# Kernel optimization log

Hardware: AMD Instinct MI355X
Metric: run time of the kernel (lower is better)

Reference implementation:

```python
import jax, jax.numpy as jnp
import numpy as np

B, S, D = 8, 1024, 1024
H = 16
DH = D // H
DFF = 4096
L = 2
EPS = 1e-6


def setup_inputs() -> dict:
    key = jax.random.key(0)
    ks = jax.random.split(key, 12)
    sc = 0.02
    x = jax.random.normal(ks[0], (B, S, D), dtype=jnp.float32)
    # causal mask: 1 where position j > i (masked), broadcast over batch/head
    mask = jnp.triu(jnp.ones((S, S), dtype=jnp.float32), k=1)[None, None]
    Wq = jax.random.normal(ks[1], (L, D, D), dtype=jnp.float32) * sc
    Wk = jax.random.normal(ks[2], (L, D, D), dtype=jnp.float32) * sc
    Wv = jax.random.normal(ks[3], (L, D, D), dtype=jnp.float32) * sc
    Wo = jax.random.normal(ks[4], (L, D, D), dtype=jnp.float32) * sc
    bq = jnp.zeros((L, D), jnp.float32)
    bk = jnp.zeros((L, D), jnp.float32)
    bv = jnp.zeros((L, D), jnp.float32)
    bo = jnp.zeros((L, D), jnp.float32)
    W1 = jax.random.normal(ks[5], (L, D, DFF), dtype=jnp.float32) * sc
    b1 = jnp.zeros((L, DFF), jnp.float32)
    W2 = jax.random.normal(ks[6], (L, DFF, D), dtype=jnp.float32) * sc
    b2 = jnp.zeros((L, D), jnp.float32)
    ln1_g = jnp.ones((L, D), jnp.float32)
    ln1_b = jnp.zeros((L, D), jnp.float32)
    ln2_g = jnp.ones((L, D), jnp.float32)
    ln2_b = jnp.zeros((L, D), jnp.float32)
    return dict(x=x, mask=mask, Wq=Wq, bq=bq, Wk=Wk, bk=bk, Wv=Wv, bv=bv,
                Wo=Wo, bo=bo, W1=W1, b1=b1, W2=W2, b2=b2,
                ln1_g=ln1_g, ln1_b=ln1_b, ln2_g=ln2_g, ln2_b=ln2_b)


def layer_norm(x, g, b):
    mu = jnp.mean(x, axis=-1, keepdims=True)
    var = jnp.mean(jnp.square(x - mu), axis=-1, keepdims=True)
    return (x - mu) * jax.lax.rsqrt(var + EPS) * g + b


def reference(x, mask, Wq, bq, Wk, bk, Wv, bv, Wo, bo, W1, b1, W2, b2,
              ln1_g, ln1_b, ln2_g, ln2_b):
    scale = 1.0 / jnp.sqrt(jnp.float32(DH))
    for l in range(L):
        # --- multi-head attention (inference mode: no dropout) ---
        q = (x @ Wq[l] + bq[l]).reshape(B, S, H, DH).transpose(0, 2, 1, 3)
        k = (x @ Wk[l] + bk[l]).reshape(B, S, H, DH).transpose(0, 2, 1, 3)
        v = (x @ Wv[l] + bv[l]).reshape(B, S, H, DH).transpose(0, 2, 1, 3)
        sim = jnp.einsum('bhqd,bhkd->bhqk', q, k) * scale + mask * (-1e9)
        attn = jax.nn.softmax(sim, axis=-1)
        o = jnp.einsum('bhqk,bhkd->bhqd', attn, v)
        o = o.transpose(0, 2, 1, 3).reshape(B, S, D)
        o = o @ Wo[l] + bo[l]
        x = layer_norm(o + x, ln1_g[l], ln1_b[l])
        # --- feed-forward network ---
        h = jax.nn.relu(x @ W1[l] + b1[l])
        f = h @ W2[l] + b2[l]
        x = layer_norm(x + f, ln2_g[l], ln2_b[l])
    return x
```

## Files before the change

kernel.cpp:

```cpp
#include <hip/hip_runtime.h>

typedef __attribute__((ext_vector_type(8))) short bf16x8;
typedef __attribute__((ext_vector_type(4))) float f32x4;
typedef unsigned short ushort_t;
typedef unsigned int uint32;

#define DEV __device__ __forceinline__

DEV ushort_t f2bf(float f) {
    uint32 u = __float_as_uint(f);
    uint32 r = (u + 0x7FFFu + ((u >> 16) & 1u)) >> 16;
    return (ushort_t)r;
}

#define MFMA16(a, b, c) __builtin_amdgcn_mfma_f32_16x16x32_bf16((a), (b), (c), 0, 0, 0)

DEV void gload_lds16(const void* g, void* l) {
    __builtin_amdgcn_global_load_lds((const __attribute__((address_space(1))) void*)g,
                                     (__attribute__((address_space(3))) void*)l,
                                     16, 0, 0);
}

__global__ __launch_bounds__(256) void init_x(const float* __restrict__ xin,
                                              float* __restrict__ x,
                                              ushort_t* __restrict__ xb, int n4) {
    int i = blockIdx.x * 256 + threadIdx.x;
    if (i >= n4) return;
    float4 v = ((const float4*)xin)[i];
    ((float4*)x)[i] = v;
    ushort4 h;
    h.x = f2bf(v.x); h.y = f2bf(v.y); h.z = f2bf(v.z); h.w = f2bf(v.w);
    ((ushort4*)xb)[i] = h;
}

__global__ __launch_bounds__(256) void transpose_convert(const float* __restrict__ src,
                                                         ushort_t* __restrict__ dst,
                                                         int K, int N) {
    __shared__ float tile[32][33];
    int tx = threadIdx.x, ty = threadIdx.y;
    int nt = blockIdx.x * 32, kt = blockIdx.y * 32;
#pragma unroll
    for (int j = 0; j < 4; ++j)
        tile[ty + j * 8][tx] = src[(size_t)(kt + ty + j * 8) * N + nt + tx];
    __syncthreads();
#pragma unroll
    for (int j = 0; j < 4; ++j)
        dst[(size_t)(nt + ty + j * 8) * K + kt + tx] = f2bf(tile[tx][ty + j * 8]);
}

template <int BM, int MODE, int RELU>
__global__ __launch_bounds__(512, 2) void gemm8p(const ushort_t* __restrict__ A,
                                                 const ushort_t* __restrict__ BT,
                                                 const float* __restrict__ bias,
                                                 void* __restrict__ Cout,
                                                 int M, int N, int K, int gx,
                                                 ushort_t* __restrict__ qout,
                                                 ushort_t* __restrict__ kout,
                                                 ushort_t* __restrict__ vtout,
                                                 const float* __restrict__ bq,
                                                 const float* __restrict__ bk,
                                                 const float* __restrict__ bv) {
    constexpr int AH = BM / 128;
    constexpr int MREP = BM / 32;
    constexpr int MPP = MREP / 4;
    __shared__ ushort_t lds[2][(BM + 256) * 64];

    const int nwg = gridDim.x;
    const int q8 = nwg >> 3, r8 = nwg & 7;
    const int xcd = blockIdx.x & 7, idx = blockIdx.x >> 3;
    const int swz = (xcd < r8 ? xcd * (q8 + 1) : r8 * (q8 + 1) + (xcd - r8) * q8) + idx;
    const int bxi = swz % gx, byi = swz / gx;

    const int tid = threadIdx.x;
    const int w = tid >> 6, lane = tid & 63;
    const int wr = w >> 2, wc = w & 3;
    const int lr = lane & 15, lh = lane >> 4;
    const int row0 = byi * BM, col0 = bxi * 256;

    f32x4 acc[MREP][4] = {};

    const ushort_t* __restrict__ Ab = A + (size_t)row0 * K;
    const ushort_t* __restrict__ Bb = BT + (size_t)col0 * K;
    const int nt = K >> 6;

    const int sr8 = lane & 7;
    const int r8l = lane >> 3;
    const int cu = (lane & 7) ^ r8l;

    auto stage_half = [&](const ushort_t* src, ushort_t* lbase) {
#pragma unroll
        for (int i = 0; i < 2; ++i) {
            const int rowi = (w * 2 + i) * 8 + r8l;
            gload_lds16(src + (size_t)rowi * K + cu * 8, lbase + (w * 2 + i) * 512 + lane * 8);
        }
    };
    auto Ahalf = [&](int buf, int h) -> ushort_t* { return &lds[buf][h * 8192]; };
    auto Bhalf = [&](int buf, int h) -> ushort_t* { return &lds[buf][BM * 64 + h * 8192]; };
    auto stA = [&](int kt, int h, int buf) {
        stage_half(Ab + (size_t)h * 128 * K + (size_t)kt * 64, Ahalf(buf, h));
    };
    auto stB = [&](int kt, int h, int buf) {
        stage_half(Bb + (size_t)h * 128 * K + (size_t)kt * 64, Bhalf(buf, h));
    };

    stB(0, 0, 0); stB(0, 1, 0);
    stA(0, 0, 0); if (AH == 2) stA(0, 1, 0);
    stB(1, 0, 1); stB(1, 1, 1);
    asm volatile("s_waitcnt vmcnt(4)" ::: "memory");
    __builtin_amdgcn_sched_barrier(0);
    __builtin_amdgcn_s_barrier();

    for (int t = 0; t < nt; ++t) {
        const int cb = t & 1, nb = cb ^ 1;
        bf16x8 bfrag[4][2];
#pragma unroll
        for (int p = 0; p < 4; ++p) {
            if (p == 0) {
#pragma unroll
                for (int ni = 0; ni < 4; ++ni) {
                    const int br = wc * 64 + ni * 16 + lr;
                    const ushort_t* bh = Bhalf(cb, br >> 7);
                    const int rr = br & 127;
#pragma unroll
                    for (int ks = 0; ks < 2; ++ks)
                        bfrag[ni][ks] = *(const bf16x8*)&bh[rr * 64 + (((ks * 4 + lh) ^ (rr & 7)) * 8)];
                }
            }
            bf16x8 af[MPP][2];
#pragma unroll
            for (int mm = 0; mm < MPP; ++mm) {
                const int fr = wr * (BM / 2) + (p * MPP + mm) * 16 + lr;
                const ushort_t* ah = Ahalf(cb, fr >> 7);
                const int rr = fr & 127;
#pragma unroll
                for (int ks = 0; ks < 2; ++ks)
                    af[mm][ks] = *(const bf16x8*)&ah[rr * 64 + (((ks * 4 + lh) ^ (rr & 7)) * 8)];
            }
            if (p == 0) { if (t + 1 < nt) stA(t + 1, 0, nb); }
            else if (p == 1) { if (AH == 2 && t + 1 < nt) stA(t + 1, 1, nb); }
            else if (p == 2) { if (t + 2 < nt) stB(t + 2, 0, cb); }
            else {
                if (t + 2 < nt) {
                    stB(t + 2, 1, cb);
                    asm volatile("s_waitcnt vmcnt(4)" ::: "memory");
                } else if (t + 1 < nt) {
                    asm volatile("s_waitcnt vmcnt(0)" ::: "memory");
                }
            }
            __builtin_amdgcn_sched_barrier(0);
            __builtin_amdgcn_s_barrier();
            asm volatile("s_waitcnt lgkmcnt(0)" ::: "memory");
            __builtin_amdgcn_sched_barrier(0);
            __builtin_amdgcn_s_setprio(1);
#pragma unroll
            for (int mm = 0; mm < MPP; ++mm)
#pragma unroll
                for (int ni = 0; ni < 4; ++ni)
#pragma unroll
                    for (int ks = 0; ks < 2; ++ks)
                        acc[p * MPP + mm][ni] = MFMA16(af[mm][ks], bfrag[ni][ks], acc[p * MPP + mm][ni]);
            __builtin_amdgcn_s_setprio(0);
            __builtin_amdgcn_sched_barrier(0);
            __builtin_amdgcn_s_barrier();
        }
    }
    (void)sr8; (void)M;

#pragma unroll
    for (int mi = 0; mi < MREP; ++mi) {
#pragma unroll
        for (int ni = 0; ni < 4; ++ni) {
            const int col = col0 + wc * 64 + ni * 16 + lr;
            const int rowb = row0 + wr * (BM / 2) + mi * 16 + lh * 4;
            if (MODE == 2) {
                if (col < 1024) {
                    const float bvv = bq[col];
#pragma unroll
                    for (int r = 0; r < 4; ++r)
                        qout[(size_t)(rowb + r) * 1024 + col] = f2bf((acc[mi][ni][r] + bvv) * 0.125f);
                } else if (col < 2048) {
                    const int c = col - 1024;
                    const float bvv = bk[c];
#pragma unroll
                    for (int r = 0; r < 4; ++r)
                        kout[(size_t)(rowb + r) * 1024 + c] = f2bf(acc[mi][ni][r] + bvv);
                } else {
                    const int d = col - 2048;
                    const int h = d >> 6, dd = d & 63;
                    const int b = rowb >> 10, s = rowb & 1023;
                    const float bvv = bv[d];
                    ushort4 h4;
                    h4.x = f2bf(acc[mi][ni][0] + bvv);
                    h4.y = f2bf(acc[mi][ni][1] + bvv);
                    h4.z = f2bf(acc[mi][ni][2] + bvv);
                    h4.w = f2bf(acc[mi][ni][3] + bvv);
                    *(ushort4*)&vtout[(((size_t)(b * 16 + h) * 64 + dd) << 10) + s] = h4;
                }
            } else {
                const float bvv = bias[col];
#pragma unroll
                for (int r = 0; r < 4; ++r) {
                    float val = acc[mi][ni][r] + bvv;
                    if (RELU) val = fmaxf(val, 0.f);
                    if (MODE == 1)
                        ((ushort_t*)Cout)[(size_t)(rowb + r) * N + col] = f2bf(val);
                    else
                        ((float*)Cout)[(size_t)(rowb + r) * N + col] = val;
                }
            }
        }
    }
}

__global__ __launch_bounds__(256) void attn_kernel(const ushort_t* __restrict__ q,
                                                   const ushort_t* __restrict__ k,
                                                   const ushort_t* __restrict__ vt,
                                                   ushort_t* __restrict__ o) {
    __shared__ ushort_t ktile[64 * 64];
    __shared__ ushort_t vtile[64 * 64];
    __shared__ ushort_t p_lds[4][16 * 64];

    const int bh = blockIdx.x;
    const int b = bh >> 4, h = bh & 15;
    const int qt = blockIdx.y;
    const int tid = threadIdx.x, w = tid >> 6, lane = tid & 63;
    const int lr = lane & 15, lh = lane >> 4;
    const int qbase = qt * 64 + w * 16;
    const size_t headoff = (size_t)b * 1024 * 1024 + h * 64;
    const size_t vhead = (size_t)(b * 16 + h) << 16;

    bf16x8 qf[2];
#pragma unroll
    for (int ks = 0; ks < 2; ++ks)
        qf[ks] = *(const bf16x8*)&q[headoff + (size_t)(qbase + lr) * 1024 + ks * 32 + lh * 8];

    f32x4 oacc[4] = {};
    float m[4] = {-INFINITY, -INFINITY, -INFINITY, -INFINITY};
    float ls[4] = {0.f, 0.f, 0.f, 0.f};

    const int srow = tid >> 3;
    const int scolb = (tid & 7) * 16;
    const int swz0 = ((srow & 7) << 4);
    char* const kbase = (char*)ktile;
    char* const vbase = (char*)vtile;
    char* const kw0 = kbase + srow * 128 + (scolb ^ swz0);
    char* const kw1 = kbase + (srow + 32) * 128 + (scolb ^ swz0);
    char* const vw0 = vbase + srow * 128 + (scolb ^ swz0);
    char* const vw1 = vbase + (srow + 32) * 128 + (scolb ^ swz0);
    const ushort_t* kg = k + headoff + (size_t)srow * 1024 + (tid & 7) * 8;
    const ushort_t* vg = vt + vhead + (size_t)srow * 1024 + (tid & 7) * 8;

    const int jmaxw = qbase + 15;
    const int jend = qt * 64 + 63;

    bf16x8 sk0 = *(const bf16x8*)&kg[0];
    bf16x8 sk1 = *(const bf16x8*)&kg[32 * 1024];
    bf16x8 sv0 = *(const bf16x8*)&vg[0];
    bf16x8 sv1 = *(const bf16x8*)&vg[32 * 1024];

    for (int j0 = 0; j0 <= jend; j0 += 64) {
        __syncthreads();
        *(bf16x8*)kw0 = sk0;
        *(bf16x8*)kw1 = sk1;
        *(bf16x8*)vw0 = sv0;
        *(bf16x8*)vw1 = sv1;
        __syncthreads();
        if (j0 + 64 <= jend) {
            sk0 = *(const bf16x8*)&kg[(size_t)(j0 + 64) * 1024];
            sk1 = *(const bf16x8*)&kg[(size_t)(j0 + 64) * 1024 + 32 * 1024];
            sv0 = *(const bf16x8*)&vg[j0 + 64];
            sv1 = *(const bf16x8*)&vg[32 * 1024 + j0 + 64];
        }

        if (j0 <= jmaxw) {
            f32x4 s[4] = {{0,0,0,0},{0,0,0,0},{0,0,0,0},{0,0,0,0}};
#pragma unroll
            for (int kt = 0; kt < 4; ++kt) {
                const int row = kt * 16 + lr;
                const int rswz = ((row & 7) << 4);
#pragma unroll
                for (int ks = 0; ks < 2; ++ks) {
                    bf16x8 kf = *(const bf16x8*)(kbase + row * 128 + ((ks * 64 + lh * 16) ^ rswz));
                    s[kt] = MFMA16(qf[ks], kf, s[kt]);
                }
            }
            if (j0 + 63 > qbase) {
#pragma unroll
                for (int kt = 0; kt < 4; ++kt)
#pragma unroll
                    for (int r = 0; r < 4; ++r)
                        s[kt][r] = ((j0 + kt * 16 + lr) <= (qbase + lh * 4 + r)) ? s[kt][r] : -1e9f;
            }
#pragma unroll
            for (int r = 0; r < 4; ++r) {
                float pm = fmaxf(fmaxf(s[0][r], s[1][r]), fmaxf(s[2][r], s[3][r]));
                pm = fmaxf(pm, __shfl_xor(pm, 1, 16));
                pm = fmaxf(pm, __shfl_xor(pm, 2, 16));
                pm = fmaxf(pm, __shfl_xor(pm, 4, 16));
                pm = fmaxf(pm, __shfl_xor(pm, 8, 16));
                const float mn = fmaxf(m[r], pm);
                const float corr = __expf(m[r] - mn);
                m[r] = mn;
                float p0 = __expf(s[0][r] - mn);
                float p1 = __expf(s[1][r] - mn);
                float p2 = __expf(s[2][r] - mn);
                float p3 = __expf(s[3][r] - mn);
                s[0][r] = p0; s[1][r] = p1; s[2][r] = p2; s[3][r] = p3;
                float ps = (p0 + p1) + (p2 + p3);
                ps += __shfl_xor(ps, 1, 16);
                ps += __shfl_xor(ps, 2, 16);
                ps += __shfl_xor(ps, 4, 16);
                ps += __shfl_xor(ps, 8, 16);
                ls[r] = ls[r] * corr + ps;
                oacc[0][r] *= corr; oacc[1][r] *= corr;
                oacc[2][r] *= corr; oacc[3][r] *= corr;
            }
            char* const pb = (char*)p_lds[w];
#pragma unroll
            for (int r = 0; r < 4; ++r) {
                const int qrow = lh * 4 + r;
                const int qswz = ((qrow & 7) << 4);
#pragma unroll
                for (int kt = 0; kt < 4; ++kt)
                    *(ushort_t*)(pb + qrow * 128 + ((kt * 32 + lr * 2) ^ qswz)) = f2bf(s[kt][r]);
            }
            const int pswz = ((lr & 7) << 4);
            bf16x8 pa0 = *(const bf16x8*)(pb + lr * 128 + ((lh * 16) ^ pswz));
            bf16x8 pa1 = *(const bf16x8*)(pb + lr * 128 + ((64 + lh * 16) ^ pswz));
#pragma unroll
            for (int dt = 0; dt < 4; ++dt) {
                const int vrow = dt * 16 + lr;
                const int vswz = ((vrow & 7) << 4);
                bf16x8 vf0 = *(const bf16x8*)(vbase + vrow * 128 + ((lh * 16) ^ vswz));
                oacc[dt] = MFMA16(pa0, vf0, oacc[dt]);
                bf16x8 vf1 = *(const bf16x8*)(vbase + vrow * 128 + ((64 + lh * 16) ^ vswz));
                oacc[dt] = MFMA16(pa1, vf1, oacc[dt]);
            }
        }
    }

    float inv[4];
#pragma unroll
    for (int r = 0; r < 4; ++r) inv[r] = 1.f / ls[r];
#pragma unroll
    for (int dt = 0; dt < 4; ++dt)
#pragma unroll
        for (int r = 0; r < 4; ++r) {
            const int row = qbase + lh * 4 + r;
            o[headoff + (size_t)row * 1024 + dt * 16 + lr] = f2bf(oacc[dt][r] * inv[r]);
        }
}

__global__ __launch_bounds__(256) void add_ln(const float* __restrict__ t,
                                              float* __restrict__ x,
                                              const float* __restrict__ g,
                                              const float* __restrict__ bb,
                                              ushort_t* __restrict__ xb) {
    const int row = blockIdx.x, tid = threadIdx.x;
    const int lane = tid & 63, w = tid >> 6;
    const size_t base = (size_t)row * 1024;
    float4 tv = ((const float4*)(t + base))[tid];
    float4 xv = ((const float4*)(x + base))[tid];
    float v0 = tv.x + xv.x, v1 = tv.y + xv.y, v2 = tv.z + xv.z, v3 = tv.w + xv.w;
    float s = v0 + v1 + v2 + v3;
    float sq = v0 * v0 + v1 * v1 + v2 * v2 + v3 * v3;
#pragma unroll
    for (int off = 32; off >= 1; off >>= 1) {
        s += __shfl_xor(s, off);
        sq += __shfl_xor(sq, off);
    }
    __shared__ float red[8];
    if (lane == 0) { red[w] = s; red[4 + w] = sq; }
    __syncthreads();
    s = red[0] + red[1] + red[2] + red[3];
    sq = red[4] + red[5] + red[6] + red[7];
    const float mu = s * (1.f / 1024.f);
    const float var = sq * (1.f / 1024.f) - mu * mu;
    const float rs = rsqrtf(var + 1e-6f);
    float4 gv = ((const float4*)g)[tid];
    float4 bv = ((const float4*)bb)[tid];
    float y0 = (v0 - mu) * rs * gv.x + bv.x;
    float y1 = (v1 - mu) * rs * gv.y + bv.y;
    float y2 = (v2 - mu) * rs * gv.z + bv.z;
    float y3 = (v3 - mu) * rs * gv.w + bv.w;
    float4 yo; yo.x = y0; yo.y = y1; yo.z = y2; yo.w = y3;
    ((float4*)(x + base))[tid] = yo;
    ushort4 hh;
    hh.x = f2bf(y0); hh.y = f2bf(y1); hh.z = f2bf(y2); hh.w = f2bf(y3);
    ((ushort4*)(xb + base))[tid] = hh;
}

extern "C" void kernel_launch(void* const* d_in, const int* in_sizes, int n_in,
                              void* d_out, int out_size, void* d_ws, size_t ws_size,
                              hipStream_t stream) {
    (void)in_sizes; (void)n_in; (void)out_size; (void)ws_size;
    const int B = 8, S = 1024, D = 1024, DFF = 4096, L = 2;
    const int M = B * S;

    const float* x_in = (const float*)d_in[0];
    const float* Wq = (const float*)d_in[2];
    const float* bq = (const float*)d_in[3];
    const float* Wk = (const float*)d_in[4];
    const float* bk = (const float*)d_in[5];
    const float* Wv = (const float*)d_in[6];
    const float* bv = (const float*)d_in[7];
    const float* Wo = (const float*)d_in[8];
    const float* bo = (const float*)d_in[9];
    const float* W1 = (const float*)d_in[10];
    const float* b1 = (const float*)d_in[11];
    const float* W2 = (const float*)d_in[12];
    const float* b2 = (const float*)d_in[13];
    const float* ln1g = (const float*)d_in[14];
    const float* ln1b = (const float*)d_in[15];
    const float* ln2g = (const float*)d_in[16];
    const float* ln2b = (const float*)d_in[17];

    float* x = (float*)d_out;
    char* ws = (char*)d_ws;
    const size_t MB = 1024 * 1024;
    ushort_t* wqkvT = (ushort_t*)(ws + 0 * MB);
    ushort_t* woT = (ushort_t*)(ws + 12 * MB);
    ushort_t* w1T = (ushort_t*)(ws + 16 * MB);
    ushort_t* w2T = (ushort_t*)(ws + 32 * MB);
    ushort_t* xb  = (ushort_t*)(ws + 48 * MB);
    ushort_t* qb  = (ushort_t*)(ws + 64 * MB);
    ushort_t* kb  = (ushort_t*)(ws + 80 * MB);
    ushort_t* vtb = (ushort_t*)(ws + 96 * MB);
    ushort_t* ob  = (ushort_t*)(ws + 112 * MB);
    ushort_t* hb  = (ushort_t*)(ws + 64 * MB);
    float* t      = (float*)(ws + 128 * MB);

    init_x<<<M * D / 4 / 256, 256, 0, stream>>>(x_in, x, xb, M * D / 4);

    dim3 tb(32, 8);
    for (int l = 0; l < L; ++l) {
        const size_t wOff = (size_t)l * D * D;
        const size_t qkvOff = (size_t)l * 3 * D * D;
        transpose_convert<<<dim3(D / 32, D / 32), tb, 0, stream>>>(Wq + wOff, wqkvT + qkvOff, D, D);
        transpose_convert<<<dim3(D / 32, D / 32), tb, 0, stream>>>(Wk + wOff, wqkvT + qkvOff + (size_t)D * D, D, D);
        transpose_convert<<<dim3(D / 32, D / 32), tb, 0, stream>>>(Wv + wOff, wqkvT + qkvOff + 2 * (size_t)D * D, D, D);
        transpose_convert<<<dim3(D / 32, D / 32), tb, 0, stream>>>(Wo + wOff, woT + wOff, D, D);
        transpose_convert<<<dim3(DFF / 32, D / 32), tb, 0, stream>>>(W1 + (size_t)l * D * DFF, w1T + (size_t)l * D * DFF, D, DFF);
        transpose_convert<<<dim3(D / 32, DFF / 32), tb, 0, stream>>>(W2 + (size_t)l * DFF * D, w2T + (size_t)l * DFF * D, DFF, D);
    }

    for (int l = 0; l < L; ++l) {
        const size_t wOff = (size_t)l * D * D;
        const size_t bOff = (size_t)l * D;
        gemm8p<256, 2, 0><<<dim3(384), 512, 0, stream>>>(
            xb, wqkvT + (size_t)l * 3 * D * D, nullptr, nullptr, M, 3 * D, D, 12,
            qb, kb, vtb, bq + bOff, bk + bOff, bv + bOff);
        attn_kernel<<<dim3(B * 16, S / 64), 256, 0, stream>>>(qb, kb, vtb, ob);
        gemm8p<128, 0, 0><<<dim3(256), 512, 0, stream>>>(
            ob, woT + wOff, bo + bOff, t, M, D, D, 4,
            nullptr, nullptr, nullptr, nullptr, nullptr, nullptr);
        add_ln<<<M, 256, 0, stream>>>(t, x, ln1g + bOff, ln1b + bOff, xb);
        gemm8p<256, 1, 1><<<dim3(512), 512, 0, stream>>>(
            xb, w1T + (size_t)l * D * DFF, b1 + (size_t)l * DFF, hb, M, DFF, D, 16,
            nullptr, nullptr, nullptr, nullptr, nullptr, nullptr);
        gemm8p<128, 0, 0><<<dim3(256), 512, 0, stream>>>(
            hb, w2T + (size_t)l * DFF * D, b2 + bOff, t, M, D, DFF, 4,
            nullptr, nullptr, nullptr, nullptr, nullptr, nullptr);
        add_ln<<<M, 256, 0, stream>>>(t, x, ln2g + bOff, ln2b + bOff, xb);
    }
}
```

Measured before the change: 768.5 us.

## Merge weight transposes, store GEMM outputs as bf16, shrink QKV GEMM tile

The twelve per-layer weight transpose launches become a single transpose_all kernel that covers every weight and layer. The output-projection and FFN-down GEMMs now write bf16 instead of fp32 into the temporary buffer, and add_ln reads bf16, which roughly halves that traffic. The QKV GEMM switches from BM=256 to BM=128 with twice the workgroups to give more parallelism. Rounding the residual branch to bf16 before layernorm adds precision loss.

```diff
diff --git a/kernel.cpp b/kernel.cpp
--- a/kernel.cpp
+++ b/kernel.cpp
@@ -12,6 +12,7 @@
     uint32 r = (u + 0x7FFFu + ((u >> 16) & 1u)) >> 16;
     return (ushort_t)r;
 }
+DEV float bf2f(ushort_t h) { return __uint_as_float(((uint32)h) << 16); }
 
 #define MFMA16(a, b, c) __builtin_amdgcn_mfma_f32_16x16x32_bf16((a), (b), (c), 0, 0, 0)
 
@@ -33,19 +34,48 @@
     ((ushort4*)xb)[i] = h;
 }
 
-__global__ __launch_bounds__(256) void transpose_convert(const float* __restrict__ src,
-                                                         ushort_t* __restrict__ dst,
-                                                         int K, int N) {
-    __shared__ float tile[32][33];
-    int tx = threadIdx.x, ty = threadIdx.y;
-    int nt = blockIdx.x * 32, kt = blockIdx.y * 32;
+__global__ __launch_bounds__(256) void transpose_all(const float* __restrict__ Wq,
+                                                     const float* __restrict__ Wk,
+                                                     const float* __restrict__ Wv,
+                                                     const float* __restrict__ Wo,
+                                                     const float* __restrict__ W1,
+                                                     const float* __restrict__ W2,
+                                                     ushort_t* __restrict__ wqkvT,
+                                                     ushort_t* __restrict__ woT,
+                                                     ushort_t* __restrict__ w1T,
+                                                     ushort_t* __restrict__ w2T) {
+    const int l = blockIdx.y;
+    const int t = blockIdx.x;
+    const float* src;
+    ushort_t* dst;
+    int K, N, ktile, ntile;
+    if (t < 4096) {
+        const int which = t >> 10, tile = t & 1023;
+        K = 1024; N = 1024; ktile = tile >> 5; ntile = tile & 31;
+        const size_t o1 = (size_t)l * 1048576;
+        if (which == 0)      { src = Wq + o1; dst = wqkvT + (size_t)l * 3145728; }
+        else if (which == 1) { src = Wk + o1; dst = wqkvT + (size_t)l * 3145728 + 1048576; }
+        else if (which == 2) { src = Wv + o1; dst = wqkvT + (size_t)l * 3145728 + 2097152; }
+        else                 { src = Wo + o1; dst = woT + o1; }
+    } else if (t < 8192) {
+        const int tile = t - 4096;
+        K = 1024; N = 4096; ktile = tile >> 7; ntile = tile & 127;
+        src = W1 + (size_t)l * 4194304; dst = w1T + (size_t)l * 4194304;
+    } else {
+        const int tile = t - 8192;
+        K = 4096; N = 1024; ktile = tile >> 5; ntile = tile & 31;
+        src = W2 + (size_t)l * 4194304; dst = w2T + (size_t)l * 4194304;
+    }
+    __shared__ float tilebuf[32][33];
+    const int tx = threadIdx.x, ty = threadIdx.y;
+    const int nt = ntile * 32, kt = ktile * 32;
 #pragma unroll
     for (int j = 0; j < 4; ++j)
-        tile[ty + j * 8][tx] = src[(size_t)(kt + ty + j * 8) * N + nt + tx];
+        tilebuf[ty + j * 8][tx] = src[(size_t)(kt + ty + j * 8) * N + nt + tx];
     __syncthreads();
 #pragma unroll
     for (int j = 0; j < 4; ++j)
-        dst[(size_t)(nt + ty + j * 8) * K + kt + tx] = f2bf(tile[tx][ty + j * 8]);
+        dst[(size_t)(nt + ty + j * 8) * K + kt + tx] = f2bf(tilebuf[tx][ty + j * 8]);
 }
 
 template <int BM, int MODE, int RELU>
@@ -83,7 +113,6 @@
     const ushort_t* __restrict__ Bb = BT + (size_t)col0 * K;
     const int nt = K >> 6;
 
-    const int sr8 = lane & 7;
     const int r8l = lane >> 3;
     const int cu = (lane & 7) ^ r8l;
 
@@ -164,7 +193,7 @@
             __builtin_amdgcn_s_barrier();
         }
     }
-    (void)sr8; (void)M;
+    (void)M;
 
 #pragma unroll
     for (int mi = 0; mi < MREP; ++mi) {
@@ -202,10 +231,7 @@
                 for (int r = 0; r < 4; ++r) {
                     float val = acc[mi][ni][r] + bvv;
                     if (RELU) val = fmaxf(val, 0.f);
-                    if (MODE == 1)
-                        ((ushort_t*)Cout)[(size_t)(rowb + r) * N + col] = f2bf(val);
-                    else
-                        ((float*)Cout)[(size_t)(rowb + r) * N + col] = val;
+                    ((ushort_t*)Cout)[(size_t)(rowb + r) * N + col] = f2bf(val);
                 }
             }
         }
@@ -351,7 +377,7 @@
         }
 }
 
-__global__ __launch_bounds__(256) void add_ln(const float* __restrict__ t,
+__global__ __launch_bounds__(256) void add_ln(const ushort_t* __restrict__ t,
                                               float* __restrict__ x,
                                               const float* __restrict__ g,
                                               const float* __restrict__ bb,
@@ -359,9 +385,10 @@
     const int row = blockIdx.x, tid = threadIdx.x;
     const int lane = tid & 63, w = tid >> 6;
     const size_t base = (size_t)row * 1024;
-    float4 tv = ((const float4*)(t + base))[tid];
+    ushort4 tv = ((const ushort4*)(t + base))[tid];
     float4 xv = ((const float4*)(x + base))[tid];
-    float v0 = tv.x + xv.x, v1 = tv.y + xv.y, v2 = tv.z + xv.z, v3 = tv.w + xv.w;
+    float v0 = bf2f(tv.x) + xv.x, v1 = bf2f(tv.y) + xv.y;
+    float v2 = bf2f(tv.z) + xv.z, v3 = bf2f(tv.w) + xv.w;
     float s = v0 + v1 + v2 + v3;
     float sq = v0 * v0 + v1 * v1 + v2 * v2 + v3 * v3;
 #pragma unroll
@@ -428,39 +455,29 @@
     ushort_t* vtb = (ushort_t*)(ws + 96 * MB);
     ushort_t* ob  = (ushort_t*)(ws + 112 * MB);
     ushort_t* hb  = (ushort_t*)(ws + 64 * MB);
-    float* t      = (float*)(ws + 128 * MB);
+    ushort_t* tb  = (ushort_t*)(ws + 128 * MB);
 
     init_x<<<M * D / 4 / 256, 256, 0, stream>>>(x_in, x, xb, M * D / 4);
-
-    dim3 tb(32, 8);
-    for (int l = 0; l < L; ++l) {
-        const size_t wOff = (size_t)l * D * D;
-        const size_t qkvOff = (size_t)l * 3 * D * D;
-        transpose_convert<<<dim3(D / 32, D / 32), tb, 0, stream>>>(Wq + wOff, wqkvT + qkvOff, D, D);
-        transpose_convert<<<dim3(D / 32, D / 32), tb, 0, stream>>>(Wk + wOff, wqkvT + qkvOff + (size_t)D * D, D, D);
-        transpose_convert<<<dim3(D / 32, D / 32), tb, 0, stream>>>(Wv + wOff, wqkvT + qkvOff + 2 * (size_t)D * D, D, D);
-        transpose_convert<<<dim3(D / 32, D / 32), tb, 0, stream>>>(Wo + wOff, woT + wOff, D, D);
-        transpose_convert<<<dim3(DFF / 32, D / 32), tb, 0, stream>>>(W1 + (size_t)l * D * DFF, w1T + (size_t)l * D * DFF, D, DFF);
-        transpose_convert<<<dim3(D / 32, DFF / 32), tb, 0, stream>>>(W2 + (size_t)l * DFF * D, w2T + (size_t)l * DFF * D, DFF, D);
-    }
+    transpose_all<<<dim3(12288, L), dim3(32, 8), 0, stream>>>(
+        Wq, Wk, Wv, Wo, W1, W2, wqkvT, woT, w1T, w2T);
 
     for (int l = 0; l < L; ++l) {
         const size_t wOff = (size_t)l * D * D;
         const size_t bOff = (size_t)l * D;
-        gemm8p<256, 2, 0><<<dim3(384), 512, 0, stream>>>(
+        gemm8p<128, 2, 0><<<dim3(768), 512, 0, stream>>>(
             xb, wqkvT + (size_t)l * 3 * D * D, nullptr, nullptr, M, 3 * D, D, 12,
             qb, kb, vtb, bq + bOff, bk + bOff, bv + bOff);
         attn_kernel<<<dim3(B * 16, S / 64), 256, 0, stream>>>(qb, kb, vtb, ob);
-        gemm8p<128, 0, 0><<<dim3(256), 512, 0, stream>>>(
-            ob, woT + wOff, bo + bOff, t, M, D, D, 4,
+        gemm8p<128, 1, 0><<<dim3(256), 512, 0, stream>>>(
+            ob, woT + wOff, bo + bOff, tb, M, D, D, 4,
             nullptr, nullptr, nullptr, nullptr, nullptr, nullptr);
-        add_ln<<<M, 256, 0, stream>>>(t, x, ln1g + bOff, ln1b + bOff, xb);
+        add_ln<<<M, 256, 0, stream>>>(tb, x, ln1g + bOff, ln1b + bOff, xb);
         gemm8p<256, 1, 1><<<dim3(512), 512, 0, stream>>>(
             xb, w1T + (size_t)l * D * DFF, b1 + (size_t)l * DFF, hb, M, DFF, D, 16,
             nullptr, nullptr, nullptr, nullptr, nullptr, nullptr);
-        gemm8p<128, 0, 0><<<dim3(256), 512, 0, stream>>>(
-            hb, w2T + (size_t)l * DFF * D, b2 + bOff, t, M, D, DFF, 4,
+        gemm8p<128, 1, 0><<<dim3(256), 512, 0, stream>>>(
+            hb, w2T + (size_t)l * DFF * D, b2 + bOff, tb, M, D, DFF, 4,
             nullptr, nullptr, nullptr, nullptr, nullptr, nullptr);
-        add_ln<<<M, 256, 0, stream>>>(t, x, ln2g + bOff, ln2b + bOff, xb);
-    }
-}
+        add_ln<<<M, 256, 0, stream>>>(tb, x, ln2g + bOff, ln2b + bOff, xb);
+    }
+}
```

Measured after the change: 735.3 us. -4.3%, faster.
